# Kernel tuning notes

Hardware: AMD Instinct MI355X
Metric: run time of the kernel (lower is better)

The kernel has to match this reference:

```python
import jax, jax.numpy as jnp
import numpy as np

D_MODEL = 1024
N_STATE = 16
D_INNER = 2 * D_MODEL          # 2048
DT_RANK = (D_MODEL + 15) // 16  # 64 = ceil(d/16)
K_CONV = 4
B, L = 1, 1024


def setup_inputs() -> dict:
    key = jax.random.key(0)
    ks = jax.random.split(key, 9)
    s = lambda fan_in: 1.0 / np.sqrt(fan_in)
    x = jax.random.normal(ks[0], (B, L, D_MODEL), dtype=jnp.float32)
    W_in = jax.random.normal(ks[1], (D_MODEL, 2 * D_INNER), dtype=jnp.float32) * s(D_MODEL)
    conv_w = jax.random.normal(ks[2], (D_INNER, K_CONV), dtype=jnp.float32) * s(K_CONV)
    conv_b = jnp.zeros((D_INNER,), dtype=jnp.float32)
    W_x = jax.random.normal(ks[3], (D_INNER, DT_RANK + 2 * N_STATE), dtype=jnp.float32) * s(D_INNER)
    W_dt = jax.random.normal(ks[4], (DT_RANK, D_INNER), dtype=jnp.float32) * s(DT_RANK)
    b_dt = jax.random.normal(ks[5], (D_INNER,), dtype=jnp.float32) * 0.01
    # A_log initialized as log(1..N) repeated over d_inner, as in __init__
    A_log = jnp.log(jnp.broadcast_to(jnp.arange(1, N_STATE + 1, dtype=jnp.float32), (D_INNER, N_STATE)))
    D = jnp.ones((D_INNER,), dtype=jnp.float32)
    W_out = jax.random.normal(ks[6], (D_INNER, D_MODEL), dtype=jnp.float32) * s(D_INNER)
    return {"x": x, "W_in": W_in, "conv_w": conv_w, "conv_b": conv_b,
            "W_x": W_x, "W_dt": W_dt, "b_dt": b_dt, "A_log": A_log,
            "D": D, "W_out": W_out}


def _causal_dw_conv(x, w, b):
    # x: [B,L,C], w: [C,K], b: [C]; causal depthwise conv (pad left K-1)
    K = w.shape[1]
    xp = jnp.pad(x, ((0, 0), (K - 1, 0), (0, 0)))
    Lx = x.shape[1]
    out = b
    for k in range(K):  # small fixed K=4
        out = out + xp[:, k:k + Lx, :] * w[:, k]
    return out


def _selective_scan(u, delta, A, Bm, Cm, D):
    # u,delta: [B,L,Di]; A: [Di,N]; Bm,Cm: [B,L,N]; D: [Di]
    dA = jnp.exp(delta[..., None] * A)                      # [B,L,Di,N]
    dBu = delta[..., None] * Bm[:, :, None, :] * u[..., None]
    dA_t = jnp.moveaxis(dA, 1, 0)    # [L,B,Di,N]
    dBu_t = jnp.moveaxis(dBu, 1, 0)
    C_t = jnp.moveaxis(Cm, 1, 0)     # [L,B,N]

    def step(h, inp):
        dA_i, dBu_i, C_i = inp
        h = dA_i * h + dBu_i
        y = jnp.einsum('bdn,bn->bd', h, C_i)
        return h, y

    h0 = jnp.zeros(u.shape[:1] + A.shape, dtype=u.dtype)  # [B,Di,N]
    _, ys = jax.lax.scan(step, h0, (dA_t, dBu_t, C_t))
    y = jnp.moveaxis(ys, 0, 1)       # [B,L,Di]
    return y + u * D


def reference(x, W_in, conv_w, conv_b, W_x, W_dt, b_dt, A_log, D, W_out):
    silu = jax.nn.silu
    x_and_res = x @ W_in                                   # [B,L,2*Di]
    x_in, res = jnp.split(x_and_res, 2, axis=-1)
    x_conv = silu(_causal_dw_conv(x_in, conv_w, conv_b))   # [B,L,Di]
    x_dbl = x_conv @ W_x                                   # [B,L,dt_rank+2N]
    dt, Bm, Cm = jnp.split(x_dbl, [DT_RANK, DT_RANK + N_STATE], axis=-1)
    delta = jax.nn.softplus(dt @ W_dt + b_dt)              # [B,L,Di]
    A = -jnp.exp(A_log)                                    # [Di,N]
    y = _selective_scan(x_conv, delta, A, Bm, Cm, D)
    return (y * silu(res)) @ W_out                         # [B,L,d_model]
```

## Files before the change

kernel.cpp:

```cpp
#include <hip/hip_runtime.h>

typedef unsigned short u16;
typedef unsigned int u32;
typedef __attribute__((ext_vector_type(8))) short bf16x8;
typedef __attribute__((ext_vector_type(4))) float f32x4;

#define LSEQ 1024

__device__ __forceinline__ float b2f(u16 v) { return __uint_as_float(((u32)v) << 16); }
__device__ __forceinline__ u16 f2b(float f) {
    u32 x = __float_as_uint(f);
    return (u16)((x + 0x7fffu + ((x >> 16) & 1u)) >> 16);
}
__device__ __forceinline__ float rdf(const void* p, size_t i, int f) {
    return f ? b2f(((const u16*)p)[i]) : ((const float*)p)[i];
}
__device__ __forceinline__ float fsig(float x) {
    return __builtin_amdgcn_rcpf(1.f + __expf(-x));
}

typedef const __attribute__((address_space(1))) u32* gp_t;
typedef __attribute__((address_space(3))) u32* lp_t;
__device__ __forceinline__ void gload16(const u16* g, u16* lds_wave_base) {
    __builtin_amdgcn_global_load_lds((gp_t)g, (lp_t)lds_wave_base, 16, 0, 0);
}

__global__ __launch_bounds__(256) void prep_k(const void* __restrict__ x,
                                              const void* __restrict__ W_in,
                                              const void* __restrict__ W_out,
                                              const void* __restrict__ W_x,
                                              const void* __restrict__ W_dt,
                                              u16* __restrict__ xb,
                                              u16* __restrict__ W_in_t,
                                              u16* __restrict__ W_out_t,
                                              u16* __restrict__ W_x_t,
                                              u16* __restrict__ W_dt_t,
                                              int* __restrict__ flag) {
    __shared__ int cnt;
    __shared__ __align__(8) u16 tile[32][36];
    if (threadIdx.x == 0) cnt = 0;
    __syncthreads();
    const u16* xu = (const u16*)x;
    int c = 0;
#pragma unroll
    for (int j = 0; j < 8; ++j) {
        u16 u = xu[threadIdx.x * 8 + j];
        int e = (u >> 7) & 0xFF;
        c += (e == 0 || (e >= 100 && e <= 140)) ? 1 : 0;
    }
    atomicAdd(&cnt, c);
    __syncthreads();
    const int f = (cnt >= 1638) ? 1 : 0;
    if (blockIdx.x == 0 && threadIdx.x == 0) *flag = f;

    int blk = blockIdx.x;
    if (blk < 1024) {
        int i = (blk * 256 + threadIdx.x) * 4;
        ushort4 o;
        if (f) {
            o = *(const ushort4*)(xu + i);
        } else {
            float4 v = *(const float4*)((const float*)x + i);
            o = make_ushort4(f2b(v.x), f2b(v.y), f2b(v.z), f2b(v.w));
        }
        *(ushort4*)(xb + i) = o;
        return;
    }
    blk -= 1024;
    const void* src; u16* dst; int R, Cn, nbc, t;
    if (blk < 4096)      { src = W_in;  dst = W_in_t;  R = 1024; Cn = 4096; nbc = 128; t = blk; }
    else if (blk < 6144) { src = W_out; dst = W_out_t; R = 2048; Cn = 1024; nbc = 32;  t = blk - 4096; }
    else if (blk < 6400) { src = W_x;   dst = W_x_t;   R = 2048; Cn = 96;   nbc = 4;   t = blk - 6144; }
    else                 { src = W_dt;  dst = W_dt_t;  R = 64;   Cn = 2048; nbc = 64;  t = blk - 6400; }
    int br = t / nbc, bc = t - br * nbc;
    int r0 = br * 32, c0 = bc * 32;
    {
        int ty = threadIdx.x >> 3, tx4 = (threadIdx.x & 7) << 2;
        u16 o0 = 0, o1 = 0, o2 = 0, o3 = 0;
        if (c0 + tx4 < Cn) {
            size_t off = (size_t)(r0 + ty) * Cn + c0 + tx4;
            if (f) {
                ushort4 u = *(const ushort4*)((const u16*)src + off);
                o0 = u.x; o1 = u.y; o2 = u.z; o3 = u.w;
            } else {
                float4 v = *(const float4*)((const float*)src + off);
                o0 = f2b(v.x); o1 = f2b(v.y); o2 = f2b(v.z); o3 = f2b(v.w);
            }
        }
        *(ushort4*)(&tile[ty][tx4]) = make_ushort4(o0, o1, o2, o3);
    }
    __syncthreads();
    {
        int cc = threadIdx.x >> 3, r4 = (threadIdx.x & 7) << 2;
        ushort4 o = make_ushort4(tile[r4][cc], tile[r4 + 1][cc], tile[r4 + 2][cc], tile[r4 + 3][cc]);
        *(ushort4*)(dst + (size_t)(c0 + cc) * R + r0 + r4) = o;
    }
}

template <int MT, int NT, int OUT_MODE>
__global__ __launch_bounds__(256) void gemm_bt(const u16* __restrict__ A,
                                               const u16* __restrict__ Bt,
                                               void* __restrict__ C,
                                               int M, int N, int K,
                                               const int* __restrict__ flag) {
    constexpr int BM = 32 * MT, BN = 32 * NT;
    __shared__ __align__(16) u16 As[BM * 32];
    __shared__ __align__(16) u16 Bs[BN * 32];
    const int tid = threadIdx.x;
    const int w = tid >> 6, lane = tid & 63;
    const int wm = w & 1, wn = w >> 1;
    const int m_blk = blockIdx.x * BM, n_blk = blockIdx.y * BN;
    const int lm = lane & 15, lq = lane >> 4;
    const int sr = lane >> 2, sc = (lane & 3) << 3;
    const int f = (OUT_MODE == 2) ? flag[0] : 0;

    f32x4 acc[MT][NT];
#pragma unroll
    for (int i = 0; i < MT; ++i)
#pragma unroll
        for (int j = 0; j < NT; ++j) acc[i][j] = (f32x4){0.f, 0.f, 0.f, 0.f};

    for (int kb = 0; kb < K; kb += 32) {
        __syncthreads();
#pragma unroll
        for (int i = 0; i < BM / 64; ++i) {
            int row = i * 64 + w * 16;
            gload16(A + (size_t)(m_blk + row + sr) * K + kb + sc, As + row * 32);
        }
#pragma unroll
        for (int i = 0; i < BN / 64; ++i) {
            int row = i * 64 + w * 16;
            gload16(Bt + (size_t)(n_blk + row + sr) * K + kb + sc, Bs + row * 32);
        }
        __syncthreads();

        bf16x8 af[MT], bf[NT];
#pragma unroll
        for (int tm = 0; tm < MT; ++tm)
            af[tm] = *(const bf16x8*)(As + (wm * 16 * MT + tm * 16 + lm) * 32 + lq * 8);
#pragma unroll
        for (int tn = 0; tn < NT; ++tn)
            bf[tn] = *(const bf16x8*)(Bs + (wn * 16 * NT + tn * 16 + lm) * 32 + lq * 8);
#pragma unroll
        for (int tm = 0; tm < MT; ++tm)
#pragma unroll
            for (int tn = 0; tn < NT; ++tn)
                acc[tm][tn] = __builtin_amdgcn_mfma_f32_16x16x32_bf16(af[tm], bf[tn],
                                                                      acc[tm][tn], 0, 0, 0);
    }

#pragma unroll
    for (int tm = 0; tm < MT; ++tm)
#pragma unroll
        for (int tn = 0; tn < NT; ++tn)
#pragma unroll
            for (int r = 0; r < 4; ++r) {
                int row = m_blk + wm * 16 * MT + tm * 16 + lq * 4 + r;
                int col = n_blk + wn * 16 * NT + tn * 16 + lm;
                float v = acc[tm][tn][r];
                if (OUT_MODE == 1) {
                    ((u16*)C)[(size_t)row * N + col] = f2b(v);
                } else {
                    if (f) ((u16*)C)[(size_t)row * N + col] = f2b(v);
                    else   ((float*)C)[(size_t)row * N + col] = v;
                }
            }
}

__global__ __launch_bounds__(256) void gemm2_conv_k(const u16* __restrict__ xz,
                                                    const u16* __restrict__ Bt,
                                                    float* __restrict__ parts,
                                                    u16* __restrict__ xconv,
                                                    const void* __restrict__ cw,
                                                    const void* __restrict__ cb,
                                                    const int* __restrict__ flag) {
    constexpr int MT = 2, NT = 4;
    constexpr int BM = 64, BN = 128, K = 2048, KLEN = 256;
    __shared__ __align__(16) u16 As[BM * 32];
    __shared__ __align__(16) u16 Bs[BN * 32];
    __shared__ __align__(16) float cws[KLEN * 4];
    __shared__ float cbs[KLEN];
    const int tid = threadIdx.x;
    const int w = tid >> 6, lane = tid & 63;
    const int wm = w & 1, wn = w >> 1;
    const int m_blk = blockIdx.x * BM;
    const int kb0 = blockIdx.z * KLEN;
    const int lm = lane & 15, lq = lane >> 4;
    const int sr = lane >> 2, sc = (lane & 3) << 3;
    const int f = flag[0];

    {
#pragma unroll
        for (int k = 0; k < 4; ++k) cws[tid * 4 + k] = rdf(cw, (size_t)(kb0 + tid) * 4 + k, f);
        cbs[tid] = rdf(cb, kb0 + tid, f);
    }

    f32x4 acc[MT][NT];
#pragma unroll
    for (int i = 0; i < MT; ++i)
#pragma unroll
        for (int j = 0; j < NT; ++j) acc[i][j] = (f32x4){0.f, 0.f, 0.f, 0.f};

    const int arow = tid >> 2;
    const int acg = (tid & 3) << 3;
    const int trow = m_blk + arow;

    for (int kb = kb0; kb < kb0 + KLEN; kb += 32) {
        __syncthreads();
        {
            const int d = kb + acg;
            const int dl = kb - kb0 + acg;
            bf16x8 xv[4];
#pragma unroll
            for (int kk = 0; kk < 4; ++kk) {
                bf16x8 zz = {0, 0, 0, 0, 0, 0, 0, 0};
                int tt = trow + kk - 3;
                xv[kk] = (tt >= 0) ? *(const bf16x8*)(xz + (size_t)tt * 4096 + d) : zz;
            }
            bf16x8 rv;
#pragma unroll
            for (int j = 0; j < 8; ++j) {
                f32x4 wv = *(const f32x4*)(cws + (dl + j) * 4);
                float a = cbs[dl + j];
#pragma unroll
                for (int kk = 0; kk < 4; ++kk) a += b2f((u16)xv[kk][j]) * wv[kk];
                rv[j] = (short)f2b(a * fsig(a));
            }
            *(bf16x8*)(As + arow * 32 + acg) = rv;
            *(bf16x8*)(xconv + (size_t)trow * 2048 + d) = rv;
        }
#pragma unroll
        for (int i = 0; i < BN / 64; ++i) {
            int row = i * 64 + w * 16;
            gload16(Bt + (size_t)(row + sr) * K + kb + sc, Bs + row * 32);
        }
        __syncthreads();

        bf16x8 af[MT], bf[NT];
#pragma unroll
        for (int tm = 0; tm < MT; ++tm)
            af[tm] = *(const bf16x8*)(As + (wm * 32 + tm * 16 + lm) * 32 + lq * 8);
#pragma unroll
        for (int tn = 0; tn < NT; ++tn)
            bf[tn] = *(const bf16x8*)(Bs + (wn * 64 + tn * 16 + lm) * 32 + lq * 8);
#pragma unroll
        for (int tm = 0; tm < MT; ++tm)
#pragma unroll
            for (int tn = 0; tn < NT; ++tn)
                acc[tm][tn] = __builtin_amdgcn_mfma_f32_16x16x32_bf16(af[tm], bf[tn],
                                                                      acc[tm][tn], 0, 0, 0);
    }
#pragma unroll
    for (int tm = 0; tm < MT; ++tm)
#pragma unroll
        for (int tn = 0; tn < NT; ++tn)
#pragma unroll
            for (int r = 0; r < 4; ++r) {
                int row = m_blk + wm * 32 + tm * 16 + lq * 4 + r;
                int col = wn * 64 + tn * 16 + lm;
                parts[(size_t)blockIdx.z * 131072 + (size_t)row * 128 + col] = acc[tm][tn][r];
            }
}

__global__ __launch_bounds__(256) void gemm3_red_k(const float* __restrict__ parts,
                                                   const u16* __restrict__ Bt,
                                                   float* __restrict__ delta,
                                                   const void* __restrict__ bias,
                                                   const int* __restrict__ flag) {
    constexpr int MT = 2, NT = 2, BM = 64, BN = 64, K = 64;
    __shared__ __align__(16) u16 As[BM * 32];
    __shared__ __align__(16) u16 Bs[BN * 32];
    const int tid = threadIdx.x;
    const int w = tid >> 6, lane = tid & 63;
    const int wm = w & 1, wn = w >> 1;
    const int m_blk = blockIdx.x * BM, n_blk = blockIdx.y * BN;
    const int lm = lane & 15, lq = lane >> 4;
    const int sr = lane >> 2, sc = (lane & 3) << 3;
    const int f = flag[0];

    f32x4 acc[MT][NT];
#pragma unroll
    for (int i = 0; i < MT; ++i)
#pragma unroll
        for (int j = 0; j < NT; ++j) acc[i][j] = (f32x4){0.f, 0.f, 0.f, 0.f};

    const int arow = tid >> 2;
    const int acg = (tid & 3) << 3;

    for (int kb = 0; kb < K; kb += 32) {
        __syncthreads();
        {
            f32x4 s0 = {0.f, 0.f, 0.f, 0.f}, s1 = {0.f, 0.f, 0.f, 0.f};
#pragma unroll
            for (int sl = 0; sl < 8; ++sl) {
                const float* p = parts + (size_t)sl * 131072 + (size_t)(m_blk + arow) * 128 + kb + acg;
                s0 += *(const f32x4*)p;
                s1 += *(const f32x4*)(p + 4);
            }
            bf16x8 rv;
#pragma unroll
            for (int j = 0; j < 4; ++j) {
                rv[j] = (short)f2b(s0[j]);
                rv[4 + j] = (short)f2b(s1[j]);
            }
            *(bf16x8*)(As + arow * 32 + acg) = rv;
        }
        {
            int row = w * 16;
            gload16(Bt + (size_t)(n_blk + row + sr) * K + kb + sc, Bs + row * 32);
        }
        __syncthreads();

        bf16x8 af[MT], bf[NT];
#pragma unroll
        for (int tm = 0; tm < MT; ++tm)
            af[tm] = *(const bf16x8*)(As + (wm * 32 + tm * 16 + lm) * 32 + lq * 8);
#pragma unroll
        for (int tn = 0; tn < NT; ++tn)
            bf[tn] = *(const bf16x8*)(Bs + (wn * 32 + tn * 16 + lm) * 32 + lq * 8);
#pragma unroll
        for (int tm = 0; tm < MT; ++tm)
#pragma unroll
            for (int tn = 0; tn < NT; ++tn)
                acc[tm][tn] = __builtin_amdgcn_mfma_f32_16x16x32_bf16(af[tm], bf[tn],
                                                                      acc[tm][tn], 0, 0, 0);
    }
#pragma unroll
    for (int tm = 0; tm < MT; ++tm)
#pragma unroll
        for (int tn = 0; tn < NT; ++tn)
#pragma unroll
            for (int r = 0; r < 4; ++r) {
                int row = m_blk + wm * 32 + tm * 16 + lq * 4 + r;
                int col = n_blk + wn * 32 + tn * 16 + lm;
                float b = rdf(bias, col, f);
                float t2 = acc[tm][tn][r] + b;
                float sp = fmaxf(t2, 0.f) + __logf(1.f + __expf(-fabsf(t2)));
                delta[(size_t)row * 2048 + col] = sp;
            }
}

__global__ __launch_bounds__(256) void scan1_k(const float* __restrict__ delta,
                                               const u16* __restrict__ xc,
                                               const float* __restrict__ parts,
                                               const void* __restrict__ A_log,
                                               float* __restrict__ Acar,
                                               float* __restrict__ Bcar,
                                               const int* __restrict__ flag) {
    __shared__ float BCs[32][32];
    const int f = *flag;
    const int g = blockIdx.x * 256 + threadIdx.x;
    const int c = g >> 12, rem = g & 4095;
    const int d = rem >> 1, nh = rem & 1;
    const int n0 = nh << 3;
    const int t0 = c * 32;
    {
        int idx = threadIdx.x * 4;
        int tl = idx >> 5, col = idx & 31;
        f32x4 s = {0.f, 0.f, 0.f, 0.f};
#pragma unroll
        for (int sl = 0; sl < 8; ++sl)
            s += *(const f32x4*)(parts + (size_t)sl * 131072 + (size_t)(t0 + tl) * 128 + 64 + col);
        *(f32x4*)&BCs[tl][col] = s;
    }
    __syncthreads();

    float A[8], P[8], h[8];
#pragma unroll
    for (int j = 0; j < 8; ++j) {
        A[j] = -__expf(rdf(A_log, d * 16 + n0 + j, f));
        P[j] = 1.f;
        h[j] = 0.f;
    }
#pragma unroll 4
    for (int i = 0; i < 32; ++i) {
        int t = t0 + i;
        float de = delta[t * 2048 + d];
        float dBu = de * b2f(xc[t * 2048 + d]);
        f32x4 Bv0 = *(const f32x4*)&BCs[i][n0];
        f32x4 Bv1 = *(const f32x4*)&BCs[i][n0 + 4];
#pragma unroll
        for (int j = 0; j < 8; ++j) {
            float Bv = (j < 4) ? Bv0[j & 3] : Bv1[j & 3];
            float a = __expf(de * A[j]);
            h[j] = a * h[j] + Bv * dBu;
            P[j] *= a;
        }
    }
    f32x4 pa0 = {P[0], P[1], P[2], P[3]}, pa1 = {P[4], P[5], P[6], P[7]};
    f32x4 hb0 = {h[0], h[1], h[2], h[3]}, hb1 = {h[4], h[5], h[6], h[7]};
    size_t base = (size_t)c * 32768 + d * 16 + n0;
    *(f32x4*)(Acar + base) = pa0;
    *(f32x4*)(Acar + base + 4) = pa1;
    *(f32x4*)(Bcar + base) = hb0;
    *(f32x4*)(Bcar + base + 4) = hb1;
}

__global__ __launch_bounds__(64) void scan2_k(const float* __restrict__ Acar,
                                              float* __restrict__ Bcar) {
    int idx = blockIdx.x * 64 + threadIdx.x;
    float a[32], b[32];
#pragma unroll
    for (int c = 0; c < 32; ++c) {
        a[c] = Acar[c * 32768 + idx];
        b[c] = Bcar[c * 32768 + idx];
    }
    float H = 0.f;
#pragma unroll
    for (int c = 0; c < 32; ++c) {
        float t = b[c];
        b[c] = H;
        H = a[c] * H + t;
    }
#pragma unroll
    for (int c = 0; c < 32; ++c) Bcar[c * 32768 + idx] = b[c];
}

__global__ __launch_bounds__(256) void scan3_k(const float* __restrict__ delta,
                                               const u16* __restrict__ xc,
                                               const float* __restrict__ parts,
                                               const u16* __restrict__ xz,
                                               const void* __restrict__ A_log,
                                               const void* __restrict__ Dvp,
                                               const float* __restrict__ Bcar,
                                               u16* __restrict__ yg,
                                               const int* __restrict__ flag) {
    __shared__ float BCs[32][32];
    const int f = *flag;
    const int g = blockIdx.x * 256 + threadIdx.x;
    const int c = g >> 12, rem = g & 4095;
    const int d = rem >> 1, nh = rem & 1;
    const int n0 = nh << 3;
    const int t0 = c * 32;
    {
        int idx = threadIdx.x * 4;
        int tl = idx >> 5, col = idx & 31;
        f32x4 s = {0.f, 0.f, 0.f, 0.f};
#pragma unroll
        for (int sl = 0; sl < 8; ++sl)
            s += *(const f32x4*)(parts + (size_t)sl * 131072 + (size_t)(t0 + tl) * 128 + 64 + col);
        *(f32x4*)&BCs[tl][col] = s;
    }
    __syncthreads();

    float A[8], h[8];
    size_t base = (size_t)c * 32768 + d * 16 + n0;
    f32x4 h0 = *(const f32x4*)(Bcar + base);
    f32x4 h1 = *(const f32x4*)(Bcar + base + 4);
#pragma unroll
    for (int j = 0; j < 8; ++j) {
        A[j] = -__expf(rdf(A_log, d * 16 + n0 + j, f));
        h[j] = (j < 4) ? h0[j & 3] : h1[j & 3];
    }
    float Dd = rdf(Dvp, d, f);
#pragma unroll 4
    for (int i = 0; i < 32; ++i) {
        int t = t0 + i;
        float de = delta[t * 2048 + d];
        float u = b2f(xc[t * 2048 + d]);
        float dBu = de * u;
        f32x4 Bv0 = *(const f32x4*)&BCs[i][n0];
        f32x4 Bv1 = *(const f32x4*)&BCs[i][n0 + 4];
        f32x4 Cv0 = *(const f32x4*)&BCs[i][16 + n0];
        f32x4 Cv1 = *(const f32x4*)&BCs[i][20 + n0];
        float p = 0.f;
#pragma unroll
        for (int j = 0; j < 8; ++j) {
            float Bv = (j < 4) ? Bv0[j & 3] : Bv1[j & 3];
            float Cv = (j < 4) ? Cv0[j & 3] : Cv1[j & 3];
            float a = __expf(de * A[j]);
            h[j] = a * h[j] + Bv * dBu;
            p += h[j] * Cv;
        }
        p += __shfl_xor(p, 1);
        if (nh == 0) {
            float r = b2f(xz[(size_t)t * 4096 + 2048 + d]);
            float yt = p + u * Dd;
            yg[t * 2048 + d] = f2b(yt * r * fsig(r));
        }
    }
}

__global__ __launch_bounds__(256) void scan_k(const float* __restrict__ delta,
                                              const u16* __restrict__ xc,
                                              const float* __restrict__ parts,
                                              const u16* __restrict__ xz,
                                              const void* __restrict__ A_log,
                                              const void* __restrict__ Dvp,
                                              u16* __restrict__ yg,
                                              const int* __restrict__ flag) {
    int f = *flag;
    int g = blockIdx.x * 256 + threadIdx.x;
    int d = g >> 4, n = g & 15;
    float A = -__expf(rdf(A_log, d * 16 + n, f));
    float Dd = rdf(Dvp, d, f);
    float h = 0.f;
    for (int t = 0; t < LSEQ; ++t) {
        float de = delta[t * 2048 + d];
        float u = b2f(xc[t * 2048 + d]);
        float Bv = 0.f, Cv = 0.f;
#pragma unroll
        for (int sl = 0; sl < 8; ++sl) {
            Bv += parts[(size_t)sl * 131072 + (size_t)t * 128 + 64 + n];
            Cv += parts[(size_t)sl * 131072 + (size_t)t * 128 + 80 + n];
        }
        h = __expf(de * A) * h + (de * Bv) * u;
        float p = h * Cv;
        p += __shfl_xor(p, 1);
        p += __shfl_xor(p, 2);
        p += __shfl_xor(p, 4);
        p += __shfl_xor(p, 8);
        if (n == 0) {
            float r = b2f(xz[(size_t)t * 4096 + 2048 + d]);
            float yt = p + u * Dd;
            yg[t * 2048 + d] = f2b(yt * r * fsig(r));
        }
    }
}

extern "C" void kernel_launch(void* const* d_in, const int* in_sizes, int n_in,
                              void* d_out, int out_size, void* d_ws, size_t ws_size,
                              hipStream_t stream) {
    const void* x      = d_in[0];
    const void* W_in   = d_in[1];
    const void* conv_w = d_in[2];
    const void* conv_b = d_in[3];
    const void* W_x    = d_in[4];
    const void* W_dt   = d_in[5];
    const void* b_dt   = d_in[6];
    const void* A_log  = d_in[7];
    const void* Dv     = d_in[8];
    const void* W_out  = d_in[9];

    char* ws = (char*)d_ws;
    u16*   xz     = (u16*)(ws);
    u16*   xconv  = (u16*)(ws + 8388608);
    float* parts  = (float*)(ws + 12582912);
    float* delta  = (float*)(ws + 17432576);
    u16*   W_in_t = (u16*)(ws + 17432576);
    u16*   yg     = (u16*)(ws + 25821184);
    u16*   xb     = (u16*)(ws + 25821184);
    u16*   W_x_t  = (u16*)(ws + 30015488);
    u16*   W_dt_t = (u16*)(ws + 30539776);
    u16*   W_out_t= (u16*)(ws + 30801920);
    int*   flag   = (int*)(ws + 34996224);
    float* Acar   = (float*)(ws + 34996352);
    float* Bcar   = (float*)(ws + 39190656);
    const bool chunked_ok = (ws_size >= 43384960);

    prep_k<<<7552, 256, 0, stream>>>(x, W_in, W_out, W_x, W_dt,
                                     xb, W_in_t, W_out_t, W_x_t, W_dt_t, flag);
    gemm_bt<2, 4, 1><<<dim3(16, 32), 256, 0, stream>>>(xb, W_in_t, (void*)xz,
                                                       1024, 4096, 1024, flag);
    gemm2_conv_k<<<dim3(16, 1, 8), 256, 0, stream>>>(xz, W_x_t, parts, xconv,
                                                     conv_w, conv_b, flag);
    gemm3_red_k<<<dim3(16, 32), 256, 0, stream>>>(parts, W_dt_t, delta, b_dt, flag);

    if (chunked_ok) {
        scan1_k<<<512, 256, 0, stream>>>(delta, xconv, parts, A_log, Acar, Bcar, flag);
        scan2_k<<<512, 64, 0, stream>>>(Acar, Bcar);
        scan3_k<<<512, 256, 0, stream>>>(delta, xconv, parts, xz, A_log, Dv, Bcar, yg, flag);
    } else {
        scan_k<<<128, 256, 0, stream>>>(delta, xconv, parts, xz, A_log, Dv, yg, flag);
    }

    gemm_bt<2, 2, 2><<<dim3(16, 16), 256, 0, stream>>>(yg, W_out_t, d_out,
                                                       1024, 1024, 2048, flag);
}
```

Baseline: 225.8 us.

## Double-buffer LDS tiles in GEMM kernels to overlap loads with MFMA

```diff
diff --git a/kernel.cpp b/kernel.cpp
--- a/kernel.cpp
+++ b/kernel.cpp
@@ -104,8 +104,8 @@
                                                int M, int N, int K,
                                                const int* __restrict__ flag) {
     constexpr int BM = 32 * MT, BN = 32 * NT;
-    __shared__ __align__(16) u16 As[BM * 32];
-    __shared__ __align__(16) u16 Bs[BN * 32];
+    __shared__ __align__(16) u16 As[2][BM * 32];
+    __shared__ __align__(16) u16 Bs[2][BN * 32];
     const int tid = threadIdx.x;
     const int w = tid >> 6, lane = tid & 63;
     const int wm = w & 1, wn = w >> 1;
@@ -120,34 +120,44 @@
 #pragma unroll
         for (int j = 0; j < NT; ++j) acc[i][j] = (f32x4){0.f, 0.f, 0.f, 0.f};
 
-    for (int kb = 0; kb < K; kb += 32) {
-        __syncthreads();
+    auto stage = [&](int buf, int kb) {
 #pragma unroll
         for (int i = 0; i < BM / 64; ++i) {
             int row = i * 64 + w * 16;
-            gload16(A + (size_t)(m_blk + row + sr) * K + kb + sc, As + row * 32);
+            gload16(A + (size_t)(m_blk + row + sr) * K + kb + sc, &As[buf][row * 32]);
         }
 #pragma unroll
         for (int i = 0; i < BN / 64; ++i) {
             int row = i * 64 + w * 16;
-            gload16(Bt + (size_t)(n_blk + row + sr) * K + kb + sc, Bs + row * 32);
-        }
-        __syncthreads();
-
+            gload16(Bt + (size_t)(n_blk + row + sr) * K + kb + sc, &Bs[buf][row * 32]);
+        }
+    };
+    auto compute = [&](int buf) {
         bf16x8 af[MT], bf[NT];
 #pragma unroll
         for (int tm = 0; tm < MT; ++tm)
-            af[tm] = *(const bf16x8*)(As + (wm * 16 * MT + tm * 16 + lm) * 32 + lq * 8);
+            af[tm] = *(const bf16x8*)(&As[buf][(wm * 16 * MT + tm * 16 + lm) * 32 + lq * 8]);
 #pragma unroll
         for (int tn = 0; tn < NT; ++tn)
-            bf[tn] = *(const bf16x8*)(Bs + (wn * 16 * NT + tn * 16 + lm) * 32 + lq * 8);
+            bf[tn] = *(const bf16x8*)(&Bs[buf][(wn * 16 * NT + tn * 16 + lm) * 32 + lq * 8]);
 #pragma unroll
         for (int tm = 0; tm < MT; ++tm)
 #pragma unroll
             for (int tn = 0; tn < NT; ++tn)
                 acc[tm][tn] = __builtin_amdgcn_mfma_f32_16x16x32_bf16(af[tm], bf[tn],
                                                                       acc[tm][tn], 0, 0, 0);
-    }
+    };
+
+    stage(0, 0);
+    __syncthreads();
+    int cur = 0;
+    for (int kb = 32; kb < K; kb += 32) {
+        stage(cur ^ 1, kb);
+        compute(cur);
+        __syncthreads();
+        cur ^= 1;
+    }
+    compute(cur);
 
 #pragma unroll
     for (int tm = 0; tm < MT; ++tm)
@@ -176,8 +186,8 @@
                                                     const int* __restrict__ flag) {
     constexpr int MT = 2, NT = 4;
     constexpr int BM = 64, BN = 128, K = 2048, KLEN = 256;
-    __shared__ __align__(16) u16 As[BM * 32];
-    __shared__ __align__(16) u16 Bs[BN * 32];
+    __shared__ __align__(16) u16 As[2][BM * 32];
+    __shared__ __align__(16) u16 Bs[2][BN * 32];
     __shared__ __align__(16) float cws[KLEN * 4];
     __shared__ float cbs[KLEN];
     const int tid = threadIdx.x;
@@ -194,6 +204,7 @@
         for (int k = 0; k < 4; ++k) cws[tid * 4 + k] = rdf(cw, (size_t)(kb0 + tid) * 4 + k, f);
         cbs[tid] = rdf(cb, kb0 + tid, f);
     }
+    __syncthreads();
 
     f32x4 acc[MT][NT];
 #pragma unroll
@@ -205,51 +216,64 @@
     const int acg = (tid & 3) << 3;
     const int trow = m_blk + arow;
 
-    for (int kb = kb0; kb < kb0 + KLEN; kb += 32) {
-        __syncthreads();
-        {
-            const int d = kb + acg;
-            const int dl = kb - kb0 + acg;
-            bf16x8 xv[4];
-#pragma unroll
-            for (int kk = 0; kk < 4; ++kk) {
-                bf16x8 zz = {0, 0, 0, 0, 0, 0, 0, 0};
-                int tt = trow + kk - 3;
-                xv[kk] = (tt >= 0) ? *(const bf16x8*)(xz + (size_t)tt * 4096 + d) : zz;
-            }
-            bf16x8 rv;
-#pragma unroll
-            for (int j = 0; j < 8; ++j) {
-                f32x4 wv = *(const f32x4*)(cws + (dl + j) * 4);
-                float a = cbs[dl + j];
-#pragma unroll
-                for (int kk = 0; kk < 4; ++kk) a += b2f((u16)xv[kk][j]) * wv[kk];
-                rv[j] = (short)f2b(a * fsig(a));
-            }
-            *(bf16x8*)(As + arow * 32 + acg) = rv;
-            *(bf16x8*)(xconv + (size_t)trow * 2048 + d) = rv;
-        }
+    auto bstage = [&](int buf, int kb) {
 #pragma unroll
         for (int i = 0; i < BN / 64; ++i) {
             int row = i * 64 + w * 16;
-            gload16(Bt + (size_t)(row + sr) * K + kb + sc, Bs + row * 32);
-        }
-        __syncthreads();
-
+            gload16(Bt + (size_t)(row + sr) * K + kb + sc, &Bs[buf][row * 32]);
+        }
+    };
+    auto astage = [&](int buf, int kb) {
+        const int d = kb + acg;
+        const int dl = kb - kb0 + acg;
+        bf16x8 xv[4];
+#pragma unroll
+        for (int kk = 0; kk < 4; ++kk) {
+            bf16x8 zz = {0, 0, 0, 0, 0, 0, 0, 0};
+            int tt = trow + kk - 3;
+            xv[kk] = (tt >= 0) ? *(const bf16x8*)(xz + (size_t)tt * 4096 + d) : zz;
+        }
+        bf16x8 rv;
+#pragma unroll
+        for (int j = 0; j < 8; ++j) {
+            f32x4 wv = *(const f32x4*)(cws + (dl + j) * 4);
+            float a = cbs[dl + j];
+#pragma unroll
+            for (int kk = 0; kk < 4; ++kk) a += b2f((u16)xv[kk][j]) * wv[kk];
+            rv[j] = (short)f2b(a * fsig(a));
+        }
+        *(bf16x8*)(&As[buf][arow * 32 + acg]) = rv;
+        *(bf16x8*)(xconv + (size_t)trow * 2048 + d) = rv;
+    };
+    auto compute = [&](int buf) {
         bf16x8 af[MT], bf[NT];
 #pragma unroll
         for (int tm = 0; tm < MT; ++tm)
-            af[tm] = *(const bf16x8*)(As + (wm * 32 + tm * 16 + lm) * 32 + lq * 8);
+            af[tm] = *(const bf16x8*)(&As[buf][(wm * 32 + tm * 16 + lm) * 32 + lq * 8]);
 #pragma unroll
         for (int tn = 0; tn < NT; ++tn)
-            bf[tn] = *(const bf16x8*)(Bs + (wn * 64 + tn * 16 + lm) * 32 + lq * 8);
+            bf[tn] = *(const bf16x8*)(&Bs[buf][(wn * 64 + tn * 16 + lm) * 32 + lq * 8]);
 #pragma unroll
         for (int tm = 0; tm < MT; ++tm)
 #pragma unroll
             for (int tn = 0; tn < NT; ++tn)
                 acc[tm][tn] = __builtin_amdgcn_mfma_f32_16x16x32_bf16(af[tm], bf[tn],
                                                                       acc[tm][tn], 0, 0, 0);
-    }
+    };
+
+    bstage(0, kb0);
+    astage(0, kb0);
+    __syncthreads();
+    int cur = 0;
+    for (int kb = kb0 + 32; kb < kb0 + KLEN; kb += 32) {
+        bstage(cur ^ 1, kb);
+        astage(cur ^ 1, kb);
+        compute(cur);
+        __syncthreads();
+        cur ^= 1;
+    }
+    compute(cur);
+
 #pragma unroll
     for (int tm = 0; tm < MT; ++tm)
 #pragma unroll
@@ -268,8 +292,8 @@
                                                    const void* __restrict__ bias,
                                                    const int* __restrict__ flag) {
     constexpr int MT = 2, NT = 2, BM = 64, BN = 64, K = 64;
-    __shared__ __align__(16) u16 As[BM * 32];
-    __shared__ __align__(16) u16 Bs[BN * 32];
+    __shared__ __align__(16) u16 As[2][BM * 32];
+    __shared__ __align__(16) u16 Bs[2][BN * 32];
     const int tid = threadIdx.x;
     const int w = tid >> 6, lane = tid & 63;
     const int wm = w & 1, wn = w >> 1;
@@ -287,44 +311,55 @@
     const int arow = tid >> 2;
     const int acg = (tid & 3) << 3;
 
-    for (int kb = 0; kb < K; kb += 32) {
-        __syncthreads();
-        {
-            f32x4 s0 = {0.f, 0.f, 0.f, 0.f}, s1 = {0.f, 0.f, 0.f, 0.f};
-#pragma unroll
-            for (int sl = 0; sl < 8; ++sl) {
-                const float* p = parts + (size_t)sl * 131072 + (size_t)(m_blk + arow) * 128 + kb + acg;
-                s0 += *(const f32x4*)p;
-                s1 += *(const f32x4*)(p + 4);
-            }
-            bf16x8 rv;
-#pragma unroll
-            for (int j = 0; j < 4; ++j) {
-                rv[j] = (short)f2b(s0[j]);
-                rv[4 + j] = (short)f2b(s1[j]);
-            }
-            *(bf16x8*)(As + arow * 32 + acg) = rv;
-        }
-        {
-            int row = w * 16;
-            gload16(Bt + (size_t)(n_blk + row + sr) * K + kb + sc, Bs + row * 32);
-        }
-        __syncthreads();
-
+    auto bstage = [&](int buf, int kb) {
+        int row = w * 16;
+        gload16(Bt + (size_t)(n_blk + row + sr) * K + kb + sc, &Bs[buf][row * 32]);
+    };
+    auto astage = [&](int buf, int kb) {
+        f32x4 s0 = {0.f, 0.f, 0.f, 0.f}, s1 = {0.f, 0.f, 0.f, 0.f};
+#pragma unroll
+        for (int sl = 0; sl < 8; ++sl) {
+            const float* p = parts + (size_t)sl * 131072 + (size_t)(m_blk + arow) * 128 + kb + acg;
+            s0 += *(const f32x4*)p;
+            s1 += *(const f32x4*)(p + 4);
+        }
+        bf16x8 rv;
+#pragma unroll
+        for (int j = 0; j < 4; ++j) {
+            rv[j] = (short)f2b(s0[j]);
+            rv[4 + j] = (short)f2b(s1[j]);
+        }
+        *(bf16x8*)(&As[buf][arow * 32 + acg]) = rv;
+    };
+    auto compute = [&](int buf) {
         bf16x8 af[MT], bf[NT];
 #pragma unroll
         for (int tm = 0; tm < MT; ++tm)
-            af[tm] = *(const bf16x8*)(As + (wm * 32 + tm * 16 + lm) * 32 + lq * 8);
+            af[tm] = *(const bf16x8*)(&As[buf][(wm * 32 + tm * 16 + lm) * 32 + lq * 8]);
 #pragma unroll
         for (int tn = 0; tn < NT; ++tn)
-            bf[tn] = *(const bf16x8*)(Bs + (wn * 32 + tn * 16 + lm) * 32 + lq * 8);
+            bf[tn] = *(const bf16x8*)(&Bs[buf][(wn * 32 + tn * 16 + lm) * 32 + lq * 8]);
 #pragma unroll
         for (int tm = 0; tm < MT; ++tm)
 #pragma unroll
             for (int tn = 0; tn < NT; ++tn)
                 acc[tm][tn] = __builtin_amdgcn_mfma_f32_16x16x32_bf16(af[tm], bf[tn],
                                                                       acc[tm][tn], 0, 0, 0);
-    }
+    };
+
+    bstage(0, 0);
+    astage(0, 0);
+    __syncthreads();
+    int cur = 0;
+    for (int kb = 32; kb < K; kb += 32) {
+        bstage(cur ^ 1, kb);
+        astage(cur ^ 1, kb);
+        compute(cur);
+        __syncthreads();
+        cur ^= 1;
+    }
+    compute(cur);
+
 #pragma unroll
     for (int tm = 0; tm < MT; ++tm)
 #pragma unroll
```

Measured after the change: 222.2 us. About the same (-1.6%).
